# Kernel optimization log

Hardware: AMD Instinct MI355X
Metric: run time of the kernel (lower is better)

The kernel has to match this reference:

```python
import jax, jax.numpy as jnp
import numpy as np

HEADS = 4
DIM_HEAD = 32
SCALE = DIM_HEAD ** (-0.5)


def setup_inputs() -> dict:
    key = jax.random.key(0)
    k1, k2, k3, k4 = jax.random.split(key, 4)
    dim = 256
    hidden = HEADS * DIM_HEAD  # 128
    x = jax.random.normal(k1, (8, dim, 48, 48), dtype=jnp.float32)
    w_qkv = jax.random.normal(k2, (3 * hidden, dim), dtype=jnp.float32) * (dim ** -0.5)
    w_out = jax.random.normal(k3, (dim, hidden), dtype=jnp.float32) * (hidden ** -0.5)
    b_out = jax.random.normal(k4, (dim,), dtype=jnp.float32) * 0.01
    return {"x": x, "w_qkv": w_qkv, "w_out": w_out, "b_out": b_out}


def reference(x, w_qkv, w_out, b_out):
    b, c, h, w = x.shape
    n = h * w
    xf = x.reshape(b, c, n)                                  # [b, c, n]
    # 1x1 Conv1d (no bias) == pointwise linear over channels
    qkv = jnp.einsum('oc,bcn->bon', w_qkv, xf)               # [b, 3*hidden, n]
    q, k, v = jnp.split(qkv, 3, axis=1)                      # each [b, hidden, n]
    def to_heads(t):
        return t.reshape(b, HEADS, DIM_HEAD, n)              # b h d n
    q, k, v = to_heads(q) * SCALE, to_heads(k), to_heads(v)
    sim = jnp.einsum('bhdi,bhdj->bhij', q, k)                # [b, h, n, n]
    attn = jax.nn.softmax(sim, axis=-1)                      # stable (max-subtracted)
    out = jnp.einsum('bhij,bhdj->bhid', attn, v)             # [b, h, n, d]
    # 'b h (x y) d -> b (h d) x y'
    out = out.transpose(0, 1, 3, 2).reshape(b, HEADS * DIM_HEAD, n)
    y = jnp.einsum('oc,bcn->bon', w_out, out) + b_out[None, :, None]
    return y.reshape(b, c, h, w)
```

## Files before the change

### kernel.cpp

```cpp
#include <hip/hip_runtime.h>
#include <math.h>

#define NB    8
#define CDIM  256
#define NN    2304
#define NH    4
#define DH    32
#define HIDC  128
#define OC3   384
#define SCALE_LOG2E 0.25503524964550864f
#define SEG   2359296
#define LSEG  73728
#define PPARTS 4
#define JCHUNK 576
#define NITER  18

typedef short  bf16x8 __attribute__((ext_vector_type(8)));
typedef float  f32x4  __attribute__((ext_vector_type(4)));

__device__ __forceinline__ unsigned short f2bf(float f) {
    union { float f; unsigned u; } a; a.f = f;
    unsigned r = a.u + 0x7fffu + ((a.u >> 16) & 1u);
    return (unsigned short)(r >> 16);
}

__device__ __forceinline__ unsigned pack_trunc(float lo, float hi) {
    union { float f; unsigned u; } a, b; a.f = lo; b.f = hi;
    return (b.u & 0xFFFF0000u) | (a.u >> 16);
}

__device__ __forceinline__ float bflo(unsigned u) {
    union { unsigned u; float f; } c; c.u = u << 16; return c.f;
}
__device__ __forceinline__ float bfhi(unsigned u) {
    union { unsigned u; float f; } c; c.u = u & 0xFFFF0000u; return c.f;
}

__global__ __launch_bounds__(256) void qkv_proj_kernel(
    const float* __restrict__ x, const float* __restrict__ w,
    unsigned short* __restrict__ qt, unsigned short* __restrict__ kt,
    unsigned short* __restrict__ vtT)
{
    __shared__ unsigned short As[128 * 40];
    __shared__ unsigned short Bs[128 * 40];
    const int Lb   = (int)blockIdx.x;
    const int xcd  = Lb & 7;
    const int t    = Lb >> 3;
    const int sel  = t % 3;
    const int gl   = t / 3;
    const int group = gl * 8 + xcd;
    const int nb   = group % 18;
    const int b    = group / 18;
    const int n0 = nb * 128;
    const int o0 = sel * 128;

    const int tid  = (int)threadIdx.x;
    const int wave = tid >> 6;
    const int lane = tid & 63;
    const int li   = lane & 15;
    const int g    = lane >> 4;
    const int wm = (wave & 1) * 64;
    const int wn = (wave >> 1) * 64;
    const float* xb = x + (size_t)b * CDIM * NN;

    const int aco = (tid & 7) * 4;
    const int aor = tid >> 3;
    const int n4  = (tid & 31) * 4;
    const int c4  = (tid >> 5) * 4;
    const int l5   = tid & 31;
    const int bkey = (l5 ^ (l5 >> 2)) & 3;
    const int bsw  = ((((tid >> 6) ^ bkey) << 1) | ((tid >> 5) & 1)) << 2;

    f32x4 acc[4][4];
#pragma unroll
    for (int i = 0; i < 4; ++i)
#pragma unroll
        for (int j = 0; j < 4; ++j) acc[i][j] = (f32x4){0.f, 0.f, 0.f, 0.f};

    float4 wv[4], xv[4];
#pragma unroll
    for (int r = 0; r < 4; ++r)
        wv[r] = *(const float4*)&w[(size_t)(o0 + aor + 32 * r) * CDIM + aco];
#pragma unroll
    for (int dd = 0; dd < 4; ++dd)
        xv[dd] = *(const float4*)&xb[(size_t)(c4 + dd) * NN + n0 + n4];

    for (int k0 = 0; k0 < CDIM; k0 += 32) {
        __syncthreads();
#pragma unroll
        for (int r = 0; r < 4; ++r) {
            uint2 pk;
            pk.x = (unsigned)f2bf(wv[r].x) | ((unsigned)f2bf(wv[r].y) << 16);
            pk.y = (unsigned)f2bf(wv[r].z) | ((unsigned)f2bf(wv[r].w) << 16);
            *(uint2*)&As[(aor + 32 * r) * 40 + aco] = pk;
        }
#pragma unroll
        for (int j = 0; j < 4; ++j) {
            uint2 pk;
            pk.x = (unsigned)f2bf(((const float*)&xv[0])[j])
                 | ((unsigned)f2bf(((const float*)&xv[1])[j]) << 16);
            pk.y = (unsigned)f2bf(((const float*)&xv[2])[j])
                 | ((unsigned)f2bf(((const float*)&xv[3])[j]) << 16);
            *(uint2*)&Bs[(n4 + j) * 40 + bsw] = pk;
        }
        __syncthreads();

        const int kn = (k0 + 32 < CDIM) ? (k0 + 32) : k0;
#pragma unroll
        for (int r = 0; r < 4; ++r)
            wv[r] = *(const float4*)&w[(size_t)(o0 + aor + 32 * r) * CDIM + kn + aco];
#pragma unroll
        for (int dd = 0; dd < 4; ++dd)
            xv[dd] = *(const float4*)&xb[(size_t)(kn + c4 + dd) * NN + n0 + n4];

        bf16x8 af[4], bfr[4];
#pragma unroll
        for (int mt = 0; mt < 4; ++mt)
            af[mt] = *(const bf16x8*)&As[(wm + mt * 16 + li) * 40 + g * 8];
#pragma unroll
        for (int nt = 0; nt < 4; ++nt) {
            const int rr = wn + nt * 16 + li;
            const int rm = rr >> 2;
            bfr[nt] = *(const bf16x8*)&Bs[rr * 40 + ((g ^ ((rm ^ (rm >> 2)) & 3)) << 3)];
        }
#pragma unroll
        for (int mt = 0; mt < 4; ++mt)
#pragma unroll
            for (int nt = 0; nt < 4; ++nt)
                acc[mt][nt] = __builtin_amdgcn_mfma_f32_16x16x32_bf16(
                    af[mt], bfr[nt], acc[mt][nt], 0, 0, 0);
    }

    if (sel < 2) {
        unsigned short* dst = (sel == 0) ? qt : kt;
        const float mul = (sel == 0) ? SCALE_LOG2E : 1.0f;
#pragma unroll
        for (int mt = 0; mt < 4; ++mt) {
            const int ob = o0 + wm + mt * 16 + g * 4;
            const int d0 = ob & 31;
            const int h  = (ob & 127) >> 5;
            const size_t bh = (size_t)(b * NH + h);
#pragma unroll
            for (int nt = 0; nt < 4; ++nt) {
                const int n = n0 + wn + nt * 16 + li;
                const f32x4 a = acc[mt][nt];
                uint2 pk;
                pk.x = (unsigned)f2bf(a[0] * mul) | ((unsigned)f2bf(a[1] * mul) << 16);
                pk.y = (unsigned)f2bf(a[2] * mul) | ((unsigned)f2bf(a[3] * mul) << 16);
                *(uint2*)&dst[(bh * NN + n) * DH + d0] = pk;
            }
        }
    } else {
#pragma unroll
        for (int mt = 0; mt < 4; ++mt) {
            const int ob = o0 + wm + mt * 16 + g * 4;
            const int d0 = ob & 31;
            const int h  = (ob & 127) >> 5;
            const size_t bh = (size_t)(b * NH + h);
#pragma unroll
            for (int nt = 0; nt < 4; ++nt) {
                const int n = n0 + wn + nt * 16 + li;
                const f32x4 a = acc[mt][nt];
#pragma unroll
                for (int r = 0; r < 4; ++r)
                    vtT[(bh * DH + d0 + r) * (size_t)NN + n] = f2bf(a[r]);
            }
        }
    }
}

__global__ __launch_bounds__(64) void attn_kernel(
    const unsigned short* __restrict__ qt, const unsigned short* __restrict__ kt,
    const unsigned short* __restrict__ vtT, unsigned short* __restrict__ Op,
    float* __restrict__ Lp)
{
    __shared__ unsigned short Pl[4][16 * 32];
    const int Lb  = (int)blockIdx.x;
    const int xcd = Lb & 7;
    const int t2  = Lb >> 3;
    const int wv  = t2 & 3;
    const int t   = t2 >> 2;
    const int ib  = t % 9;
    const int grp = (t / 9) * 8 + xcd;
    const int bh  = grp >> 2;
    const int part = grp & 3;
    const int jbeg = part * JCHUNK;

    const int tid  = (int)threadIdx.x;
    const int li   = tid & 15;
    const int g    = tid >> 4;
    const int i0   = ib * 256 + wv * 64;

    const unsigned short* qb = qt  + (size_t)bh * NN * DH;
    const unsigned short* kb = kt  + (size_t)bh * NN * DH;
    const unsigned short* vb = vtT + (size_t)bh * DH * NN;

    bf16x8 qfA = *(const bf16x8*)(qb + (size_t)(i0 + li) * DH + g * 8);
    bf16x8 qfB = *(const bf16x8*)(qb + (size_t)(i0 + 16 + li) * DH + g * 8);
    bf16x8 qfC = *(const bf16x8*)(qb + (size_t)(i0 + 32 + li) * DH + g * 8);
    bf16x8 qfD = *(const bf16x8*)(qb + (size_t)(i0 + 48 + li) * DH + g * 8);

    bf16x8 ones;
#pragma unroll
    for (int r = 0; r < 8; ++r) ones[r] = (short)0x3F80;

    f32x4 O0A = {0.f,0.f,0.f,0.f}, O1A = {0.f,0.f,0.f,0.f}, LsA = {0.f,0.f,0.f,0.f};
    f32x4 O0B = {0.f,0.f,0.f,0.f}, O1B = {0.f,0.f,0.f,0.f}, LsB = {0.f,0.f,0.f,0.f};
    f32x4 O0C = {0.f,0.f,0.f,0.f}, O1C = {0.f,0.f,0.f,0.f}, LsC = {0.f,0.f,0.f,0.f};
    f32x4 O0D = {0.f,0.f,0.f,0.f}, O1D = {0.f,0.f,0.f,0.f}, LsD = {0.f,0.f,0.f,0.f};

    unsigned short* plA = &Pl[0][0];
    unsigned short* plB = &Pl[1][0];
    unsigned short* plC = &Pl[2][0];
    unsigned short* plD = &Pl[3][0];
    const int sw  = li & 6;
    const int pw  = li * 32;
    const int wr0 = pw + ((g ^ sw) << 2);
    const int wr1 = pw + (((4 + g) ^ sw) << 2);
    const int rdo = pw + (((2 * g) ^ sw) << 2);

    const unsigned short* kp0 = kb + (size_t)(jbeg + li) * DH + g * 8;
    const unsigned short* kp1 = kp0 + 16 * DH;
    const unsigned short* vp0 = vb + (size_t)li * NN + jbeg + g * 8;
    const unsigned short* vp1 = vp0 + 16 * NN;

    bf16x8 kf0A = *(const bf16x8*)kp0;
    bf16x8 kf1A = *(const bf16x8*)kp1;
    bf16x8 vf0A = *(const bf16x8*)vp0;
    bf16x8 vf1A = *(const bf16x8*)vp1;
    bf16x8 kf0B = *(const bf16x8*)(kp0 + 32 * DH);
    bf16x8 kf1B = *(const bf16x8*)(kp1 + 32 * DH);
    bf16x8 vf0B = *(const bf16x8*)(vp0 + 32);
    bf16x8 vf1B = *(const bf16x8*)(vp1 + 32);
    kp0 += 64 * DH; kp1 += 64 * DH;
    vp0 += 64;      vp1 += 64;

#define ATTN_ITER(KF0, KF1, VF0, VF1)                                          \
    do {                                                                       \
        f32x4 z = {0.f, 0.f, 0.f, 0.f};                                        \
        f32x4 s0A = __builtin_amdgcn_mfma_f32_16x16x32_bf16(KF0, qfA, z, 0, 0, 0); \
        f32x4 s0B = __builtin_amdgcn_mfma_f32_16x16x32_bf16(KF0, qfB, z, 0, 0, 0); \
        f32x4 s0C = __builtin_amdgcn_mfma_f32_16x16x32_bf16(KF0, qfC, z, 0, 0, 0); \
        f32x4 s0D = __builtin_amdgcn_mfma_f32_16x16x32_bf16(KF0, qfD, z, 0, 0, 0); \
        f32x4 s1A = __builtin_amdgcn_mfma_f32_16x16x32_bf16(KF1, qfA, z, 0, 0, 0); \
        f32x4 s1B = __builtin_amdgcn_mfma_f32_16x16x32_bf16(KF1, qfB, z, 0, 0, 0); \
        f32x4 s1C = __builtin_amdgcn_mfma_f32_16x16x32_bf16(KF1, qfC, z, 0, 0, 0); \
        f32x4 s1D = __builtin_amdgcn_mfma_f32_16x16x32_bf16(KF1, qfD, z, 0, 0, 0); \
                                     \
        KF0 = *(const bf16x8*)kp0;                                             \
        KF1 = *(const bf16x8*)kp1;                                             \
        kp0 += 32 * DH; kp1 += 32 * DH;                                        \
        float p0A[4], p1A[4], p0B[4], p1B[4];                                  \
        float p0C[4], p1C[4], p0D[4], p1D[4];                                  \
        _Pragma("unroll")                                                      \
        for (int r = 0; r < 4; ++r) {                                          \
            p0A[r] = __builtin_amdgcn_exp2f(s0A[r]);                           \
            p1A[r] = __builtin_amdgcn_exp2f(s1A[r]);                           \
            p0B[r] = __builtin_amdgcn_exp2f(s0B[r]);                           \
            p1B[r] = __builtin_amdgcn_exp2f(s1B[r]);                           \
            p0C[r] = __builtin_amdgcn_exp2f(s0C[r]);                           \
            p1C[r] = __builtin_amdgcn_exp2f(s1C[r]);                           \
            p0D[r] = __builtin_amdgcn_exp2f(s0D[r]);                           \
            p1D[r] = __builtin_amdgcn_exp2f(s1D[r]);                           \
        }                                                                      \
        uint2 wa, wb;                                                          \
        wa.x = pack_trunc(p0A[0], p0A[1]);  wa.y = pack_trunc(p0A[2], p0A[3]); \
        wb.x = pack_trunc(p1A[0], p1A[1]);  wb.y = pack_trunc(p1A[2], p1A[3]); \
        *(uint2*)&plA[wr0] = wa;                                               \
        *(uint2*)&plA[wr1] = wb;                                               \
        wa.x = pack_trunc(p0B[0], p0B[1]);  wa.y = pack_trunc(p0B[2], p0B[3]); \
        wb.x = pack_trunc(p1B[0], p1B[1]);  wb.y = pack_trunc(p1B[2], p1B[3]); \
        *(uint2*)&plB[wr0] = wa;                                               \
        *(uint2*)&plB[wr1] = wb;                                               \
        wa.x = pack_trunc(p0C[0], p0C[1]);  wa.y = pack_trunc(p0C[2], p0C[3]); \
        wb.x = pack_trunc(p1C[0], p1C[1]);  wb.y = pack_trunc(p1C[2], p1C[3]); \
        *(uint2*)&plC[wr0] = wa;                                               \
        *(uint2*)&plC[wr1] = wb;                                               \
        wa.x = pack_trunc(p0D[0], p0D[1]);  wa.y = pack_trunc(p0D[2], p0D[3]); \
        wb.x = pack_trunc(p1D[0], p1D[1]);  wb.y = pack_trunc(p1D[2], p1D[3]); \
        *(uint2*)&plD[wr0] = wa;                                               \
        *(uint2*)&plD[wr1] = wb;                                               \
        bf16x8 pfA = *(const bf16x8*)&plA[rdo];                                \
        bf16x8 pfB = *(const bf16x8*)&plB[rdo];                                \
        bf16x8 pfC = *(const bf16x8*)&plC[rdo];                                \
        bf16x8 pfD = *(const bf16x8*)&plD[rdo];                                \
        O0A = __builtin_amdgcn_mfma_f32_16x16x32_bf16(VF0,  pfA, O0A, 0, 0, 0); \
        O0B = __builtin_amdgcn_mfma_f32_16x16x32_bf16(VF0,  pfB, O0B, 0, 0, 0); \
        O0C = __builtin_amdgcn_mfma_f32_16x16x32_bf16(VF0,  pfC, O0C, 0, 0, 0); \
        O0D = __builtin_amdgcn_mfma_f32_16x16x32_bf16(VF0,  pfD, O0D, 0, 0, 0); \
        O1A = __builtin_amdgcn_mfma_f32_16x16x32_bf16(VF1,  pfA, O1A, 0, 0, 0); \
        O1B = __builtin_amdgcn_mfma_f32_16x16x32_bf16(VF1,  pfB, O1B, 0, 0, 0); \
        O1C = __builtin_amdgcn_mfma_f32_16x16x32_bf16(VF1,  pfC, O1C, 0, 0, 0); \
        O1D = __builtin_amdgcn_mfma_f32_16x16x32_bf16(VF1,  pfD, O1D, 0, 0, 0); \
        LsA = __builtin_amdgcn_mfma_f32_16x16x32_bf16(ones, pfA, LsA, 0, 0, 0); \
        LsB = __builtin_amdgcn_mfma_f32_16x16x32_bf16(ones, pfB, LsB, 0, 0, 0); \
        LsC = __builtin_amdgcn_mfma_f32_16x16x32_bf16(ones, pfC, LsC, 0, 0, 0); \
        LsD = __builtin_amdgcn_mfma_f32_16x16x32_bf16(ones, pfD, LsD, 0, 0, 0); \
                                     \
        VF0 = *(const bf16x8*)vp0;                                             \
        VF1 = *(const bf16x8*)vp1;                                             \
        vp0 += 32; vp1 += 32;                                                  \
    } while (0)

#pragma unroll 1
    for (int it = 0; it < NITER; it += 2) {
        ATTN_ITER(kf0A, kf1A, vf0A, vf1A);
        ATTN_ITER(kf0B, kf1B, vf0B, vf1B);
    }
#undef ATTN_ITER

    unsigned short* obA = Op + (size_t)part * SEG + (size_t)bh * DH * NN + i0 + li;
    unsigned short* obB = obA + 16;
    unsigned short* obC = obA + 32;
    unsigned short* obD = obA + 48;
#pragma unroll
    for (int r = 0; r < 4; ++r) {
        obA[(size_t)(4 * g + r)      * NN] = f2bf(O0A[r]);
        obA[(size_t)(16 + 4 * g + r) * NN] = f2bf(O1A[r]);
        obB[(size_t)(4 * g + r)      * NN] = f2bf(O0B[r]);
        obB[(size_t)(16 + 4 * g + r) * NN] = f2bf(O1B[r]);
        obC[(size_t)(4 * g + r)      * NN] = f2bf(O0C[r]);
        obC[(size_t)(16 + 4 * g + r) * NN] = f2bf(O1C[r]);
        obD[(size_t)(4 * g + r)      * NN] = f2bf(O0D[r]);
        obD[(size_t)(16 + 4 * g + r) * NN] = f2bf(O1D[r]);
    }
    if (g == 0) {
        float* lpb = Lp + (size_t)part * LSEG + (size_t)bh * NN + i0 + li;
        lpb[0]  = LsA[0];
        lpb[16] = LsB[0];
        lpb[32] = LsC[0];
        lpb[48] = LsD[0];
    }
}

__global__ __launch_bounds__(256) void out_proj_kernel(
    const unsigned short* __restrict__ Op, const float* __restrict__ Lp,
    const float* __restrict__ w, const float* __restrict__ bias,
    float* __restrict__ y)
{
    __shared__ unsigned short As[128 * 40];
    __shared__ unsigned short Bs[128 * 40];
    __shared__ float Linv[4][128];
    const int Lb   = (int)blockIdx.x;
    const int xcd  = Lb & 7;
    const int t    = Lb >> 3;
    const int so_  = t % 2;
    const int gl   = t / 2;
    const int group = gl * 8 + xcd;
    const int nb   = group % 18;
    const int b    = group / 18;
    const int n0 = nb * 128;
    const int o0 = so_ * 128;

    const int tid  = (int)threadIdx.x;
    const int wave = tid >> 6;
    const int lane = tid & 63;
    const int li   = lane & 15;
    const int g    = lane >> 4;
    const int wm = (wave & 1) * 64;
    const int wn = (wave >> 1) * 64;

    const int aco = (tid & 7) * 4;
    const int aor = tid >> 3;
    const int n4  = (tid & 31) * 4;
    const int d4  = (tid >> 5) * 4;
    const int l5   = tid & 31;
    const int bkey = (l5 ^ (l5 >> 2)) & 3;
    const int bsw  = ((((tid >> 6) ^ bkey) << 1) | ((tid >> 5) & 1)) << 2;

    {
        const int h = tid >> 6, nb2 = tid & 63;
#pragma unroll
        for (int half = 0; half < 2; ++half) {
            const int n = nb2 + 64 * half;
            float s = 0.f;
#pragma unroll
            for (int p = 0; p < PPARTS; ++p)
                s += Lp[(size_t)p * LSEG + (size_t)(b * NH + h) * NN + n0 + n];
            Linv[h][n] = 1.0f / s;
        }
    }

    f32x4 acc[4][4];
#pragma unroll
    for (int i = 0; i < 4; ++i)
#pragma unroll
        for (int j = 0; j < 4; ++j) acc[i][j] = (f32x4){0.f, 0.f, 0.f, 0.f};

    float4 wv[4];
    uint2  ov[PPARTS][4];
#pragma unroll
    for (int r = 0; r < 4; ++r)
        wv[r] = *(const float4*)&w[(size_t)(o0 + aor + 32 * r) * HIDC + aco];
    {
        const size_t bh0 = (size_t)(b * NH);
#pragma unroll
        for (int p = 0; p < PPARTS; ++p)
#pragma unroll
            for (int dd = 0; dd < 4; ++dd)
                ov[p][dd] = *(const uint2*)&Op[(size_t)p * SEG
                              + (bh0 * DH + d4 + dd) * (size_t)NN + n0 + n4];
    }

    for (int k0 = 0; k0 < HIDC; k0 += 32) {
        __syncthreads();
#pragma unroll
        for (int r = 0; r < 4; ++r) {
            uint2 pk;
            pk.x = (unsigned)f2bf(wv[r].x) | ((unsigned)f2bf(wv[r].y) << 16);
            pk.y = (unsigned)f2bf(wv[r].z) | ((unsigned)f2bf(wv[r].w) << 16);
            *(uint2*)&As[(aor + 32 * r) * 40 + aco] = pk;
        }
        const int h = k0 >> 5;
        {
            float s[4][4];
#pragma unroll
            for (int dd = 0; dd < 4; ++dd)
#pragma unroll
                for (int j = 0; j < 4; ++j) s[dd][j] = 0.f;
#pragma unroll
            for (int p = 0; p < PPARTS; ++p) {
#pragma unroll
                for (int dd = 0; dd < 4; ++dd) {
                    const uint2 u = ov[p][dd];
                    s[dd][0] += bflo(u.x); s[dd][1] += bfhi(u.x);
                    s[dd][2] += bflo(u.y); s[dd][3] += bfhi(u.y);
                }
            }
#pragma unroll
            for (int j = 0; j < 4; ++j) {
                const float lv = Linv[h][n4 + j];
                uint2 pk;
                pk.x = (unsigned)f2bf(s[0][j] * lv) | ((unsigned)f2bf(s[1][j] * lv) << 16);
                pk.y = (unsigned)f2bf(s[2][j] * lv) | ((unsigned)f2bf(s[3][j] * lv) << 16);
                *(uint2*)&Bs[(n4 + j) * 40 + bsw] = pk;
            }
        }
        __syncthreads();

        const int kn = (k0 + 32 < HIDC) ? (k0 + 32) : k0;
        const size_t bhn = (size_t)(b * NH + (kn >> 5));
#pragma unroll
        for (int r = 0; r < 4; ++r)
            wv[r] = *(const float4*)&w[(size_t)(o0 + aor + 32 * r) * HIDC + kn + aco];
#pragma unroll
        for (int p = 0; p < PPARTS; ++p)
#pragma unroll
            for (int dd = 0; dd < 4; ++dd)
                ov[p][dd] = *(const uint2*)&Op[(size_t)p * SEG
                              + (bhn * DH + d4 + dd) * (size_t)NN + n0 + n4];

        bf16x8 af[4], bfr[4];
#pragma unroll
        for (int mt = 0; mt < 4; ++mt)
            af[mt] = *(const bf16x8*)&As[(wm + mt * 16 + li) * 40 + g * 8];
#pragma unroll
        for (int nt = 0; nt < 4; ++nt) {
            const int rr = wn + nt * 16 + li;
            const int rm = rr >> 2;
            bfr[nt] = *(const bf16x8*)&Bs[rr * 40 + ((g ^ ((rm ^ (rm >> 2)) & 3)) << 3)];
        }
#pragma unroll
        for (int mt = 0; mt < 4; ++mt)
#pragma unroll
            for (int nt = 0; nt < 4; ++nt)
                acc[mt][nt] = __builtin_amdgcn_mfma_f32_16x16x32_bf16(
                    af[mt], bfr[nt], acc[mt][nt], 0, 0, 0);
    }

#pragma unroll
    for (int mt = 0; mt < 4; ++mt) {
        const int ob = o0 + wm + mt * 16 + g * 4;
        const float b0 = bias[ob], b1 = bias[ob + 1], b2 = bias[ob + 2], b3 = bias[ob + 3];
#pragma unroll
        for (int nt = 0; nt < 4; ++nt) {
            const int n = n0 + wn + nt * 16 + li;
            const f32x4 a = acc[mt][nt];
            float* yb = y + ((size_t)(b * CDIM + ob)) * NN + n;
            yb[0]              = a[0] + b0;
            yb[(size_t)NN]     = a[1] + b1;
            yb[(size_t)2 * NN] = a[2] + b2;
            yb[(size_t)3 * NN] = a[3] + b3;
        }
    }
}

extern "C" void kernel_launch(void* const* d_in, const int* in_sizes, int n_in,
                              void* d_out, int out_size, void* d_ws, size_t ws_size,
                              hipStream_t stream)
{
    (void)in_sizes; (void)n_in; (void)out_size; (void)ws_size;
    const float* x     = (const float*)d_in[0];
    const float* w_qkv = (const float*)d_in[1];
    const float* w_out = (const float*)d_in[2];
    const float* b_out = (const float*)d_in[3];
    float* y = (float*)d_out;

    unsigned short* qt  = (unsigned short*)d_ws;
    unsigned short* kt  = qt + SEG;
    unsigned short* vtT = kt + SEG;
    unsigned short* Op  = vtT + SEG;
    float* Lp = (float*)(Op + (size_t)PPARTS * SEG);

    qkv_proj_kernel<<<dim3(432), 256, 0, stream>>>(x, w_qkv, qt, kt, vtT);

    attn_kernel<<<dim3(4608), 64, 0, stream>>>(qt, kt, vtT, Op, Lp);

    out_proj_kernel<<<dim3(288), 256, 0, stream>>>(Op, Lp, w_out, b_out, y);
}
```

Before: 136.8 us.

## Remove split-KV partitioning in attention, process full key range per block

Drops the 4-way split of the key/value range across blocks, so each attention block now iterates over all 2304 keys and writes a single output and row-sum. The out-projection kernel no longer reads and sums four partial outputs and partial sums. This cuts partial-result traffic and reduction work. The cost is a 4x smaller grid (1152 single-wave blocks) with 4x longer loops per block, which may reduce occupancy and latency hiding on a GPU with many CUs.

New measurement: 152.8 us. +11.7%, slower.

```diff
diff --git a/kernel.cpp b/kernel.cpp
--- a/kernel.cpp
+++ b/kernel.cpp
@@ -10,10 +10,7 @@
 #define OC3   384
 #define SCALE_LOG2E 0.25503524964550864f
 #define SEG   2359296
-#define LSEG  73728
-#define PPARTS 4
-#define JCHUNK 576
-#define NITER  18
+#define NITER 72
 
 typedef short  bf16x8 __attribute__((ext_vector_type(8)));
 typedef float  f32x4  __attribute__((ext_vector_type(4)));
@@ -177,14 +174,11 @@
     __shared__ unsigned short Pl[4][16 * 32];
     const int Lb  = (int)blockIdx.x;
     const int xcd = Lb & 7;
-    const int t2  = Lb >> 3;
-    const int wv  = t2 & 3;
-    const int t   = t2 >> 2;
-    const int ib  = t % 9;
-    const int grp = (t / 9) * 8 + xcd;
-    const int bh  = grp >> 2;
-    const int part = grp & 3;
-    const int jbeg = part * JCHUNK;
+    const int t   = Lb >> 3;
+    const int wv  = t & 3;
+    const int t2  = t >> 2;
+    const int ib  = t2 % 9;
+    const int bh  = (t2 / 9) * 8 + xcd;
 
     const int tid  = (int)threadIdx.x;
     const int li   = tid & 15;
@@ -219,9 +213,9 @@
     const int wr1 = pw + (((4 + g) ^ sw) << 2);
     const int rdo = pw + (((2 * g) ^ sw) << 2);
 
-    const unsigned short* kp0 = kb + (size_t)(jbeg + li) * DH + g * 8;
+    const unsigned short* kp0 = kb + (size_t)li * DH + g * 8;
     const unsigned short* kp1 = kp0 + 16 * DH;
-    const unsigned short* vp0 = vb + (size_t)li * NN + jbeg + g * 8;
+    const unsigned short* vp0 = vb + (size_t)li * NN + g * 8;
     const unsigned short* vp1 = vp0 + 16 * NN;
 
     bf16x8 kf0A = *(const bf16x8*)kp0;
@@ -309,7 +303,7 @@
     }
 #undef ATTN_ITER
 
-    unsigned short* obA = Op + (size_t)part * SEG + (size_t)bh * DH * NN + i0 + li;
+    unsigned short* obA = Op + (size_t)bh * DH * NN + i0 + li;
     unsigned short* obB = obA + 16;
     unsigned short* obC = obA + 32;
     unsigned short* obD = obA + 48;
@@ -325,7 +319,7 @@
         obD[(size_t)(16 + 4 * g + r) * NN] = f2bf(O1D[r]);
     }
     if (g == 0) {
-        float* lpb = Lp + (size_t)part * LSEG + (size_t)bh * NN + i0 + li;
+        float* lpb = Lp + (size_t)bh * NN + i0 + li;
         lpb[0]  = LsA[0];
         lpb[16] = LsB[0];
         lpb[32] = LsC[0];
@@ -373,11 +367,7 @@
 #pragma unroll
         for (int half = 0; half < 2; ++half) {
             const int n = nb2 + 64 * half;
-            float s = 0.f;
-#pragma unroll
-            for (int p = 0; p < PPARTS; ++p)
-                s += Lp[(size_t)p * LSEG + (size_t)(b * NH + h) * NN + n0 + n];
-            Linv[h][n] = 1.0f / s;
+            Linv[h][n] = 1.0f / Lp[(size_t)(b * NH + h) * NN + n0 + n];
         }
     }
 
@@ -388,18 +378,15 @@
         for (int j = 0; j < 4; ++j) acc[i][j] = (f32x4){0.f, 0.f, 0.f, 0.f};
 
     float4 wv[4];
-    uint2  ov[PPARTS][4];
+    uint2  ov[4];
 #pragma unroll
     for (int r = 0; r < 4; ++r)
         wv[r] = *(const float4*)&w[(size_t)(o0 + aor + 32 * r) * HIDC + aco];
     {
         const size_t bh0 = (size_t)(b * NH);
 #pragma unroll
-        for (int p = 0; p < PPARTS; ++p)
-#pragma unroll
-            for (int dd = 0; dd < 4; ++dd)
-                ov[p][dd] = *(const uint2*)&Op[(size_t)p * SEG
-                              + (bh0 * DH + d4 + dd) * (size_t)NN + n0 + n4];
+        for (int dd = 0; dd < 4; ++dd)
+            ov[dd] = *(const uint2*)&Op[(bh0 * DH + d4 + dd) * (size_t)NN + n0 + n4];
     }
 
     for (int k0 = 0; k0 < HIDC; k0 += 32) {
@@ -413,26 +400,20 @@
         }
         const int h = k0 >> 5;
         {
-            float s[4][4];
-#pragma unroll
-            for (int dd = 0; dd < 4; ++dd)
-#pragma unroll
-                for (int j = 0; j < 4; ++j) s[dd][j] = 0.f;
-#pragma unroll
-            for (int p = 0; p < PPARTS; ++p) {
-#pragma unroll
-                for (int dd = 0; dd < 4; ++dd) {
-                    const uint2 u = ov[p][dd];
-                    s[dd][0] += bflo(u.x); s[dd][1] += bfhi(u.x);
-                    s[dd][2] += bflo(u.y); s[dd][3] += bfhi(u.y);
-                }
+            float s0[4], s1[4], s2[4], s3[4];
+#pragma unroll
+            for (int dd = 0; dd < 4; ++dd) {
+                const uint2 u = ov[dd];
+                s0[dd] = bflo(u.x); s1[dd] = bfhi(u.x);
+                s2[dd] = bflo(u.y); s3[dd] = bfhi(u.y);
             }
 #pragma unroll
             for (int j = 0; j < 4; ++j) {
                 const float lv = Linv[h][n4 + j];
+                const float* sj = (j == 0) ? s0 : (j == 1) ? s1 : (j == 2) ? s2 : s3;
                 uint2 pk;
-                pk.x = (unsigned)f2bf(s[0][j] * lv) | ((unsigned)f2bf(s[1][j] * lv) << 16);
-                pk.y = (unsigned)f2bf(s[2][j] * lv) | ((unsigned)f2bf(s[3][j] * lv) << 16);
+                pk.x = (unsigned)f2bf(sj[0] * lv) | ((unsigned)f2bf(sj[1] * lv) << 16);
+                pk.y = (unsigned)f2bf(sj[2] * lv) | ((unsigned)f2bf(sj[3] * lv) << 16);
                 *(uint2*)&Bs[(n4 + j) * 40 + bsw] = pk;
             }
         }
@@ -444,11 +425,8 @@
         for (int r = 0; r < 4; ++r)
             wv[r] = *(const float4*)&w[(size_t)(o0 + aor + 32 * r) * HIDC + kn + aco];
 #pragma unroll
-        for (int p = 0; p < PPARTS; ++p)
-#pragma unroll
-            for (int dd = 0; dd < 4; ++dd)
-                ov[p][dd] = *(const uint2*)&Op[(size_t)p * SEG
-                              + (bhn * DH + d4 + dd) * (size_t)NN + n0 + n4];
+        for (int dd = 0; dd < 4; ++dd)
+            ov[dd] = *(const uint2*)&Op[(bhn * DH + d4 + dd) * (size_t)NN + n0 + n4];
 
         bf16x8 af[4], bfr[4];
 #pragma unroll
@@ -500,11 +478,11 @@
     unsigned short* kt  = qt + SEG;
     unsigned short* vtT = kt + SEG;
     unsigned short* Op  = vtT + SEG;
-    float* Lp = (float*)(Op + (size_t)PPARTS * SEG);
+    float* Lp = (float*)(Op + (size_t)2 * SEG);
 
     qkv_proj_kernel<<<dim3(432), 256, 0, stream>>>(x, w_qkv, qt, kt, vtT);
 
-    attn_kernel<<<dim3(4608), 64, 0, stream>>>(qt, kt, vtT, Op, Lp);
+    attn_kernel<<<dim3(1152), 64, 0, stream>>>(qt, kt, vtT, Op, Lp);
 
     out_proj_kernel<<<dim3(288), 256, 0, stream>>>(Op, Lp, w_out, b_out, y);
 }
```
